# Performance work log

Hardware: AMD Instinct MI355X
Metric: run time of the kernel (lower is better)

Reference implementation:

```python
import jax, jax.numpy as jnp
import numpy as np

N = 100000   # nodes
E = 1600000  # edges
G = 64       # graphs
D = 64       # latent_dim
NF = 128     # num_node_feats
EF = 32      # num_edge_feats
NV = 5000    # num_node_val_feats
LV = 3       # max_lv
EPS = 1e-5


def setup_inputs() -> dict:
    key = jax.random.key(0)
    ks = jax.random.split(key, 16)
    s = 0.05
    return {
        "node_feat": jax.random.normal(ks[0], (N, NF), jnp.float32),
        "edge_feat": jax.random.normal(ks[1], (E, EF), jnp.float32),
        "w_n2l_W": jax.random.normal(ks[2], (NF, D), jnp.float32) * s,
        "w_n2l_b": jnp.zeros((D,), jnp.float32),
        "node_val_embedding": jax.random.normal(ks[3], (NV, D), jnp.float32) * s,
        "w_e2l_W": jax.random.normal(ks[4], (LV + 1, EF, D), jnp.float32) * s,
        "w_e2l_b": jnp.zeros((LV + 1, D), jnp.float32),
        "conv_W": jax.random.normal(ks[5], (LV, D, D), jnp.float32) * s,
        "conv_b": jnp.zeros((LV, D), jnp.float32),
        "l2_W": jax.random.normal(ks[6], (LV, D, D), jnp.float32) * s,
        "l2_b": jnp.zeros((LV, D), jnp.float32),
        "msg_g": jnp.ones((LV + 1, D), jnp.float32),
        "msg_b": jnp.zeros((LV + 1, D), jnp.float32),
        "hid_g": jnp.ones((LV, D), jnp.float32),
        "hid_b": jnp.zeros((LV, D), jnp.float32),
        "out_W": jax.random.normal(ks[7], (D, D), jnp.float32) * s,
        "out_b": jnp.zeros((D,), jnp.float32),
        "edge_from": jax.random.randint(ks[8], (E,), 0, N, jnp.int32),
        "edge_to": jax.random.randint(ks[9], (E,), 0, N, jnp.int32),
        "g_idx": jnp.sort(jax.random.randint(ks[10], (N,), 0, G, jnp.int32)),
        "node_val_idx": jax.random.randint(ks[11], (N,), 0, NV, jnp.int32),
    }


def _bn(x, g, b):
    # BatchNorm1d in training mode: biased batch stats
    m = jnp.mean(x, axis=0)
    v = jnp.mean(jnp.square(x - m), axis=0)
    return (x - m) * jax.lax.rsqrt(v + EPS) * g + b


def reference(node_feat, edge_feat, w_n2l_W, w_n2l_b, node_val_embedding,
              w_e2l_W, w_e2l_b, conv_W, conv_b, l2_W, l2_b,
              msg_g, msg_b, hid_g, hid_b, out_W, out_b,
              edge_from, edge_to, g_idx, node_val_idx):
    act = jax.nn.relu
    # input node transform + sparse node-value embedding (one-hot spmm == gather)
    h = node_feat @ w_n2l_W + w_n2l_b + node_val_embedding[node_val_idx]
    # edge->node pool for level 0
    e0 = edge_feat @ w_e2l_W[0] + w_e2l_b[0]
    h = h + jax.ops.segment_sum(e0, edge_to, num_segments=N)
    h = _bn(act(h), msg_g[0], msg_b[0])
    for lv in range(LV):
        # MessagePassing with add-aggr: gather sources, scatter-add to targets, then Linear
        agg = jax.ops.segment_sum(h[edge_from], edge_to, num_segments=N)
        node_linear = agg @ conv_W[lv] + conv_b[lv]
        e = edge_feat @ w_e2l_W[lv + 1] + w_e2l_b[lv + 1]
        merged = act(node_linear + jax.ops.segment_sum(e, edge_to, num_segments=N))
        merged = _bn(merged, hid_g[lv], hid_b[lv])
        h = _bn(act(merged @ l2_W[lv] + l2_b[lv] + h), msg_g[lv + 1], msg_b[lv + 1])
    # readout: gnn_out='last', readout_agg='max', act_last=True, bn=False
    pooled = jax.ops.segment_max(h, g_idx, num_segments=G)
    return act(pooled @ out_W + out_b)
```

## Files before the change

kernel.cpp:

```cpp
#include <hip/hip_runtime.h>
#include <math.h>

#define NN 100000
#define EE 1600000
#define GG 64
#define DD 64
#define NF 128
#define EF 32
#define LVL 3
#define EPSBN 1e-5f
#define NTILES ((NN + 63) / 64)
#define NBKT 391

typedef unsigned short u16;
typedef unsigned int u32;
typedef unsigned long long u64;
typedef short s4v __attribute__((ext_vector_type(4)));
typedef short bf16x8 __attribute__((ext_vector_type(8)));
typedef float f32x4 __attribute__((ext_vector_type(4)));

__device__ __forceinline__ float4 ld4(const float* p) { return *(const float4*)p; }
__device__ __forceinline__ u16 f2b(float f) {
    u32 u = __float_as_uint(f);
    return (u16)((u + 0x7FFFu + ((u >> 16) & 1u)) >> 16);
}
__device__ __forceinline__ float b2f(u16 u) { return __uint_as_float(((u32)u) << 16); }
__device__ __forceinline__ float blo(u32 u) { return __uint_as_float(u << 16); }
__device__ __forceinline__ float bhi(u32 u) { return __uint_as_float(u & 0xFFFF0000u); }

__global__ void k1b(const int* __restrict__ to, int* __restrict__ bhist) {
    __shared__ int h[NBKT];
    for (int i = threadIdx.x; i < NBKT; i += 256) h[i] = 0;
    __syncthreads();
    for (int e = blockIdx.x * 256 + threadIdx.x; e < EE; e += 256 * gridDim.x)
        atomicAdd(&h[to[e] >> 8], 1);
    __syncthreads();
    for (int i = threadIdx.x; i < NBKT; i += 256)
        if (h[i]) atomicAdd(&bhist[i], h[i]);
}

__global__ void k1c(const int* __restrict__ bhist, int* __restrict__ bbase,
                    int* __restrict__ gcur) {
    __shared__ int s[512];
    int t = threadIdx.x;
    s[t] = (t < NBKT) ? bhist[t] : 0;
    __syncthreads();
    for (int off = 1; off < 512; off <<= 1) {
        int v = (t >= off) ? s[t - off] : 0;
        __syncthreads();
        s[t] += v;
        __syncthreads();
    }
    if (t < NBKT) {
        int base = t ? s[t - 1] : 0;
        bbase[t] = base;
        gcur[t] = base;
    }
    if (t == NBKT - 1) bbase[NBKT] = s[t];
}

__global__ void k1d(const int* __restrict__ to, const int* __restrict__ from,
                    int* __restrict__ gcur, int2* __restrict__ tmp) {
    __shared__ int h[NBKT];
    __shared__ int cur[NBKT];
    for (int i = threadIdx.x; i < NBKT; i += 256) h[i] = 0;
    __syncthreads();
    for (int e = blockIdx.x * 256 + threadIdx.x; e < EE; e += 256 * gridDim.x)
        atomicAdd(&h[to[e] >> 8], 1);
    __syncthreads();
    for (int i = threadIdx.x; i < NBKT; i += 256)
        cur[i] = h[i] ? atomicAdd(&gcur[i], h[i]) : 0;
    __syncthreads();
    for (int e = blockIdx.x * 256 + threadIdx.x; e < EE; e += 256 * gridDim.x) {
        int tt = to[e];
        int b = tt >> 8;
        int pos = atomicAdd(&cur[b], 1);
        tmp[pos] = make_int2(from[e] | ((tt & 255) << 17), e);
    }
}

__global__ void kp2(const int2* __restrict__ tmp, const int* __restrict__ bbase,
                    int* __restrict__ row_ptr, int* __restrict__ src_s,
                    int* __restrict__ eid_s) {
    __shared__ int s[256];
    __shared__ int cur[256];
    int b = blockIdx.x, t = threadIdx.x;
    int e0 = bbase[b], e1 = bbase[b + 1];
    s[t] = 0;
    __syncthreads();
    for (int e = e0 + t; e < e1; e += 256) atomicAdd(&s[(tmp[e].x >> 17) & 255], 1);
    __syncthreads();
    int v = s[t];
    for (int off = 1; off < 256; off <<= 1) {
        int u = (t >= off) ? s[t - off] : 0;
        __syncthreads();
        s[t] += u;
        __syncthreads();
    }
    int excl = e0 + s[t] - v;
    cur[t] = excl;
    int n = b * 256 + t;
    if (n < NN) row_ptr[n] = excl;
    if (b == NBKT - 1 && t == 0) row_ptr[NN] = e1;
    __syncthreads();
    for (int e = e0 + t; e < e1; e += 256) {
        int2 w = tmp[e];
        int pos = atomicAdd(&cur[(w.x >> 17) & 255], 1);
        src_s[pos] = w.x & 0x1FFFF;
        eid_s[pos] = w.y;
    }
}

__global__ void kpool(const float* __restrict__ ef, const int* __restrict__ row_ptr,
                      const int* __restrict__ eid_s, u16* __restrict__ pooled) {
    int lane = threadIdx.x & 63;
    int wid = threadIdx.x >> 6;
    int w = lane & 15, slot = lane >> 4;
    for (int n = blockIdx.x * 4 + wid; n < NN; n += gridDim.x * 4) {
        int e0 = row_ptr[n], e1 = row_ptr[n + 1];
        float ax = 0.f, ay = 0.f;
        int e = e0 + slot;
        for (; e + 12 < e1; e += 16) {
            int i0 = eid_s[e], i1 = eid_s[e + 4], i2 = eid_s[e + 8], i3 = eid_s[e + 12];
            float2 v0 = *(const float2*)(ef + (size_t)i0 * EF + 2 * w);
            float2 v1 = *(const float2*)(ef + (size_t)i1 * EF + 2 * w);
            float2 v2 = *(const float2*)(ef + (size_t)i2 * EF + 2 * w);
            float2 v3 = *(const float2*)(ef + (size_t)i3 * EF + 2 * w);
            ax += (v0.x + v1.x) + (v2.x + v3.x);
            ay += (v0.y + v1.y) + (v2.y + v3.y);
        }
        for (; e < e1; e += 4) {
            float2 v = *(const float2*)(ef + (size_t)eid_s[e] * EF + 2 * w);
            ax += v.x;
            ay += v.y;
        }
        ax += __shfl_xor(ax, 16);
        ax += __shfl_xor(ax, 32);
        ay += __shfl_xor(ay, 16);
        ay += __shfl_xor(ay, 32);
        if (slot == 0) {
            u32 o = (u32)f2b(ax) | ((u32)f2b(ay) << 16);
            *(u32*)&pooled[(size_t)n * EF + 2 * w] = o;
        }
    }
}

template <int K1, int K2, bool A1BF, bool AAFF, bool EMB, bool BE, bool RESID>
__global__ __launch_bounds__(256) void kgemm_mfma(
    const void* __restrict__ A1v, const u16* __restrict__ A2,
    const float* __restrict__ W1, const float* __restrict__ W2,
    const float* __restrict__ bias, const float* __restrict__ be,
    const int* __restrict__ row_ptr, const float* __restrict__ emb,
    const int* __restrict__ nvi, const u16* __restrict__ resid,
    const float* __restrict__ raff, const float* __restrict__ aaff,
    u16* __restrict__ Xb, float* __restrict__ stats) {
    constexpr int K = K1 + K2;
    constexpr int KP = K + 8;
    __shared__ u16 A_lds[64 * KP];
    __shared__ u16 Wt_lds[64 * KP];
    __shared__ float red[128];

    const int t = threadIdx.x;
    const int lane = t & 63;
    const int wv = t >> 6;
    const int l15 = lane & 15;
    const int lg = lane >> 4;

    for (int idx = t; idx < K * 16; idx += 256) {
        int k = idx >> 4, c4 = (idx & 15) * 4;
        float4 w4 = (k < K1) ? ld4(W1 + (size_t)k * 64 + c4)
                             : ld4(W2 + (size_t)(k - K1) * 64 + c4);
        Wt_lds[(c4 + 0) * KP + k] = f2b(w4.x);
        Wt_lds[(c4 + 1) * KP + k] = f2b(w4.y);
        Wt_lds[(c4 + 2) * KP + k] = f2b(w4.z);
        Wt_lds[(c4 + 3) * KP + k] = f2b(w4.w);
    }
    if (t < 128) red[t] = 0.f;

    float bias_c[4], be_c[4], rsc_c[4], rsh_c[4];
#pragma unroll
    for (int n = 0; n < 4; n++) {
        int ch = 16 * n + l15;
        bias_c[n] = bias[ch];
        be_c[n] = BE ? be[ch] : 0.f;
        rsc_c[n] = RESID ? raff[ch] : 0.f;
        rsh_c[n] = RESID ? raff[64 + ch] : 0.f;
    }

    for (int tile = blockIdx.x; tile < NTILES; tile += gridDim.x) {
        int nb = tile * 64;
        __syncthreads();
        if (A1BF) {
            const u16* A1b = (const u16*)A1v;
            for (int idx = t; idx < 64 * (K1 / 4); idx += 256) {
                int node = idx / (K1 / 4), kq = (idx % (K1 / 4)) * 4;
                int gn = nb + node;
                s4v v = {0, 0, 0, 0};
                if (gn < NN) {
                    v = *(const s4v*)(A1b + (size_t)gn * K1 + kq);
                    if (AAFF) {
#pragma unroll
                        for (int i = 0; i < 4; i++) {
                            float f = b2f((u16)v[i]) * aaff[kq + i] + aaff[64 + kq + i];
                            v[i] = (short)f2b(f);
                        }
                    }
                }
                *(s4v*)&A_lds[node * KP + kq] = v;
            }
        } else {
            const float* A1f = (const float*)A1v;
            for (int idx = t; idx < 64 * (K1 / 4); idx += 256) {
                int node = idx / (K1 / 4), kq = (idx % (K1 / 4)) * 4;
                int gn = nb + node;
                s4v v = {0, 0, 0, 0};
                if (gn < NN) {
                    float4 a = ld4(A1f + (size_t)gn * K1 + kq);
                    v[0] = (short)f2b(a.x); v[1] = (short)f2b(a.y);
                    v[2] = (short)f2b(a.z); v[3] = (short)f2b(a.w);
                }
                *(s4v*)&A_lds[node * KP + kq] = v;
            }
        }
        if (K2 > 0) {
            for (int idx = t; idx < 64 * (K2 / 4); idx += 256) {
                int node = idx / (K2 / 4), kq = (idx % (K2 / 4)) * 4;
                int gn = nb + node;
                s4v v = {0, 0, 0, 0};
                if (gn < NN) v = *(const s4v*)(A2 + (size_t)gn * K2 + kq);
                *(s4v*)&A_lds[node * KP + K1 + kq] = v;
            }
        }
        __syncthreads();

        f32x4 acc[4];
#pragma unroll
        for (int n = 0; n < 4; n++) acc[n] = (f32x4){0.f, 0.f, 0.f, 0.f};
        const int arow = 16 * wv + l15;
#pragma unroll
        for (int kk = 0; kk < K; kk += 32) {
            s4v alo = *(const s4v*)&A_lds[arow * KP + kk + lg * 4];
            s4v ahi = *(const s4v*)&A_lds[arow * KP + kk + lg * 4 + 16];
            bf16x8 a = __builtin_shufflevector(alo, ahi, 0, 1, 2, 3, 4, 5, 6, 7);
#pragma unroll
            for (int n = 0; n < 4; n++) {
                s4v wlo = *(const s4v*)&Wt_lds[(16 * n + l15) * KP + kk + lg * 4];
                s4v whi = *(const s4v*)&Wt_lds[(16 * n + l15) * KP + kk + lg * 4 + 16];
                bf16x8 b = __builtin_shufflevector(wlo, whi, 0, 1, 2, 3, 4, 5, 6, 7);
                acc[n] = __builtin_amdgcn_mfma_f32_16x16x32_bf16(a, b, acc[n], 0, 0, 0);
            }
        }

        float ss[4] = {0, 0, 0, 0}, sq2[4] = {0, 0, 0, 0};
#pragma unroll
        for (int r = 0; r < 4; r++) {
            int node = nb + 16 * wv + lg * 4 + r;
            if (node < NN) {
                float deg = BE ? (float)(row_ptr[node + 1] - row_ptr[node]) : 0.f;
                int nv = EMB ? nvi[node] : 0;
#pragma unroll
                for (int n = 0; n < 4; n++) {
                    int ch = 16 * n + l15;
                    float v = acc[n][r] + bias_c[n];
                    if (BE) v += deg * be_c[n];
                    if (EMB) v += emb[(size_t)nv * 64 + ch];
                    if (RESID) v += b2f(resid[(size_t)node * 64 + ch]) * rsc_c[n] + rsh_c[n];
                    v = fmaxf(v, 0.f);
                    Xb[(size_t)node * 64 + ch] = f2b(v);
                    ss[n] += v;
                    sq2[n] += v * v;
                }
            }
        }
#pragma unroll
        for (int n = 0; n < 4; n++) {
            float a = ss[n];
            a += __shfl_xor(a, 16);
            a += __shfl_xor(a, 32);
            float b = sq2[n];
            b += __shfl_xor(b, 16);
            b += __shfl_xor(b, 32);
            if (lg == 0) {
                atomicAdd(&red[16 * n + l15], a);
                atomicAdd(&red[64 + 16 * n + l15], b);
            }
        }
    }
    __syncthreads();
    if (t < 128) atomicAdd(&stats[t], red[t]);
}

__global__ void kfin(float* __restrict__ stats, const float* __restrict__ g,
                     const float* __restrict__ b, int slot) {
    int t = threadIdx.x;
    float mean = stats[t] * (1.0f / NN);
    float var = stats[64 + t] * (1.0f / NN) - mean * mean;
    float rstd = rsqrtf(fmaxf(var, 0.f) + EPSBN);
    float sc = g[t] * rstd;
    float* slotp = stats + 128 + slot * 128;
    slotp[t] = sc;
    slotp[64 + t] = b[t] - mean * sc;
    stats[t] = 0.f;
    stats[64 + t] = 0.f;
}

__global__ void kmsg_bf(const u64* __restrict__ h4, const int* __restrict__ row_ptr,
                        const int* __restrict__ src_s, const float* __restrict__ aff,
                        u64* __restrict__ agg) {
    int lane = threadIdx.x & 63;
    int wid = threadIdx.x >> 6;
    int w = lane & 15, slot = lane >> 4;
    float sc0 = aff[4 * w], sc1 = aff[4 * w + 1];
    float sc2 = aff[4 * w + 2], sc3 = aff[4 * w + 3];
    float sh0 = aff[64 + 4 * w], sh1 = aff[64 + 4 * w + 1];
    float sh2 = aff[64 + 4 * w + 2], sh3 = aff[64 + 4 * w + 3];
    for (int n = blockIdx.x * 4 + wid; n < NN; n += gridDim.x * 4) {
        int e0 = row_ptr[n], e1 = row_ptr[n + 1];
        float a0 = 0.f, a1 = 0.f, a2 = 0.f, a3 = 0.f;
        int e = e0 + slot;
        for (; e + 12 < e1; e += 16) {
            int s0 = src_s[e], s1 = src_s[e + 4], s2 = src_s[e + 8], s3 = src_s[e + 12];
            u64 v0 = h4[(size_t)s0 * 16 + w];
            u64 v1 = h4[(size_t)s1 * 16 + w];
            u64 v2 = h4[(size_t)s2 * 16 + w];
            u64 v3 = h4[(size_t)s3 * 16 + w];
            u32 l0 = (u32)v0, h0 = (u32)(v0 >> 32);
            u32 l1 = (u32)v1, h1 = (u32)(v1 >> 32);
            u32 l2 = (u32)v2, h2w = (u32)(v2 >> 32);
            u32 l3 = (u32)v3, h3 = (u32)(v3 >> 32);
            a0 += (blo(l0) + blo(l1)) + (blo(l2) + blo(l3));
            a1 += (bhi(l0) + bhi(l1)) + (bhi(l2) + bhi(l3));
            a2 += (blo(h0) + blo(h1)) + (blo(h2w) + blo(h3));
            a3 += (bhi(h0) + bhi(h1)) + (bhi(h2w) + bhi(h3));
        }
        for (; e < e1; e += 4) {
            u64 v = h4[(size_t)src_s[e] * 16 + w];
            u32 l = (u32)v, h = (u32)(v >> 32);
            a0 += blo(l);
            a1 += bhi(l);
            a2 += blo(h);
            a3 += bhi(h);
        }
        a0 += __shfl_xor(a0, 16);
        a0 += __shfl_xor(a0, 32);
        a1 += __shfl_xor(a1, 16);
        a1 += __shfl_xor(a1, 32);
        a2 += __shfl_xor(a2, 16);
        a2 += __shfl_xor(a2, 32);
        a3 += __shfl_xor(a3, 16);
        a3 += __shfl_xor(a3, 32);
        if (slot == 0) {
            float deg = (float)(e1 - e0);
            u32 lo = (u32)f2b(sc0 * a0 + deg * sh0) | ((u32)f2b(sc1 * a1 + deg * sh1) << 16);
            u32 hi = (u32)f2b(sc2 * a2 + deg * sh2) | ((u32)f2b(sc3 * a3 + deg * sh3) << 16);
            agg[(size_t)n * 16 + w] = (u64)lo | ((u64)hi << 32);
        }
    }
}

__device__ __forceinline__ unsigned fenc(float f) {
    unsigned u = __float_as_uint(f);
    return (u >> 31) ? ~u : (u | 0x80000000u);
}
__device__ __forceinline__ float fdec(unsigned k) {
    return (k >> 31) ? __uint_as_float(k ^ 0x80000000u) : __uint_as_float(~k);
}

__global__ void kinitpk(unsigned* __restrict__ pk) {
    int i = blockIdx.x * blockDim.x + threadIdx.x;
    if (i < GG * DD) pk[i] = 0x007FFFFFu;
}

__global__ void kread(const u16* __restrict__ h2, const int* __restrict__ gidx,
                      const float* __restrict__ aff, unsigned* __restrict__ pk) {
    int lane = threadIdx.x & 63;
    int wid = threadIdx.x >> 6;
    float sc = aff[lane], sh = aff[64 + lane];
    int gw = blockIdx.x * 4 + wid;
    int nw = gridDim.x * 4;
    int chunk = (NN + nw - 1) / nw;
    int lo = gw * chunk, hi = min(lo + chunk, NN);
    if (lo >= hi) return;
    int cur = gidx[lo];
    float acc = -INFINITY;
    for (int n = lo; n < hi; n++) {
        int g = gidx[n];
        if (g != cur) {
            atomicMax(&pk[cur * DD + lane], fenc(acc));
            cur = g;
            acc = -INFINITY;
        }
        acc = fmaxf(acc, b2f(h2[(size_t)n * 64 + lane]) * sc + sh);
    }
    atomicMax(&pk[cur * DD + lane], fenc(acc));
}

__global__ void kout(const unsigned* __restrict__ pk, const float* __restrict__ W,
                     const float* __restrict__ b, float* __restrict__ out) {
    int t = blockIdx.x * blockDim.x + threadIdx.x;
    int g = t >> 6, d = t & 63;
    float acc = b[d];
    for (int k = 0; k < DD; k++) {
        float p = fdec(pk[g * DD + k]);
        acc += p * W[k * DD + d];
    }
    out[t] = fmaxf(acc, 0.f);
}

extern "C" void kernel_launch(void* const* d_in, const int* in_sizes, int n_in,
                              void* d_out, int out_size, void* d_ws, size_t ws_size,
                              hipStream_t stream) {
    const float* node_feat = (const float*)d_in[0];
    const float* edge_feat = (const float*)d_in[1];
    const float* w_n2l_W = (const float*)d_in[2];
    const float* w_n2l_b = (const float*)d_in[3];
    const float* nve = (const float*)d_in[4];
    const float* w_e2l_W = (const float*)d_in[5];
    const float* w_e2l_b = (const float*)d_in[6];
    const float* conv_W = (const float*)d_in[7];
    const float* conv_b = (const float*)d_in[8];
    const float* l2_W = (const float*)d_in[9];
    const float* l2_b = (const float*)d_in[10];
    const float* msg_g = (const float*)d_in[11];
    const float* msg_b = (const float*)d_in[12];
    const float* hid_g = (const float*)d_in[13];
    const float* hid_b = (const float*)d_in[14];
    const float* out_W = (const float*)d_in[15];
    const float* out_b = (const float*)d_in[16];
    const int* edge_from = (const int*)d_in[17];
    const int* edge_to = (const int*)d_in[18];
    const int* g_idx = (const int*)d_in[19];
    const int* nvi = (const int*)d_in[20];
    float* out = (float*)d_out;

    char* ws = (char*)d_ws;
    size_t off = 0;
    auto alloc = [&](size_t bytes) -> void* {
        void* p = ws + off;
        off += (bytes + 255) / 256 * 256;
        return p;
    };
    int* row_ptr = (int*)alloc((size_t)(NN + 1) * 4);
    int* src_s = (int*)alloc((size_t)EE * 4);
    int* eid_s = (int*)alloc((size_t)EE * 4);
    int2* tmp = (int2*)alloc((size_t)EE * 8);
    u16* pooled_ef = (u16*)alloc((size_t)NN * EF * 2);
    u16* h2a = (u16*)alloc((size_t)NN * DD * 2);
    u16* h2b = (u16*)alloc((size_t)NN * DD * 2);
    u16* agg_bf = (u16*)alloc((size_t)NN * DD * 2);
    u16* mb_bf = (u16*)alloc((size_t)NN * DD * 2);
    float* stats = (float*)alloc(1024 * 4);
    unsigned* pk = (unsigned*)alloc((size_t)GG * DD * 4);
    int* bhist = (int*)alloc((size_t)NBKT * 4);
    int* bbase = (int*)alloc((size_t)(NBKT + 1) * 4);
    int* gcur = (int*)alloc((size_t)NBKT * 4);
    (void)ws_size; (void)n_in; (void)in_sizes; (void)out_size;

    hipMemsetAsync(bhist, 0, (size_t)NBKT * 4, stream);
    hipMemsetAsync(stats, 0, 1024 * 4, stream);
    kinitpk<<<16, 256, 0, stream>>>(pk);

    k1b<<<256, 256, 0, stream>>>(edge_to, bhist);
    k1c<<<1, 512, 0, stream>>>(bhist, bbase, gcur);
    k1d<<<256, 256, 0, stream>>>(edge_to, edge_from, gcur, tmp);
    kp2<<<NBKT, 256, 0, stream>>>(tmp, bbase, row_ptr, src_s, eid_s);
    kpool<<<4096, 256, 0, stream>>>(edge_feat, row_ptr, eid_s, pooled_ef);

    const int GB = 782;

    kgemm_mfma<NF, EF, false, false, true, true, false>
        <<<GB, 256, 0, stream>>>(node_feat, pooled_ef, w_n2l_W, w_e2l_W,
                                 w_n2l_b, w_e2l_b, row_ptr, nve, nvi,
                                 nullptr, nullptr, nullptr, h2a, stats);
    kfin<<<1, 64, 0, stream>>>(stats, msg_g, msg_b, 0);

    u16* hcur = h2a;
    u16* hnext = h2b;
    for (int lv = 0; lv < LVL; lv++) {
        kmsg_bf<<<4096, 256, 0, stream>>>((const u64*)hcur, row_ptr, src_s,
                                          stats + 128 + lv * 128, (u64*)agg_bf);
        kgemm_mfma<DD, EF, true, false, false, true, false>
            <<<GB, 256, 0, stream>>>(agg_bf, pooled_ef, conv_W + lv * DD * DD,
                                     w_e2l_W + (size_t)(lv + 1) * EF * DD,
                                     conv_b + lv * DD,
                                     w_e2l_b + (size_t)(lv + 1) * DD, row_ptr,
                                     nullptr, nullptr, nullptr, nullptr, nullptr,
                                     mb_bf, stats);
        kfin<<<1, 64, 0, stream>>>(stats, hid_g + lv * DD, hid_b + lv * DD, 4 + lv);
        kgemm_mfma<DD, 0, true, true, false, false, true>
            <<<GB, 256, 0, stream>>>(mb_bf, nullptr, l2_W + lv * DD * DD, nullptr,
                                     l2_b + lv * DD, nullptr, row_ptr, nullptr,
                                     nullptr, hcur, stats + 128 + lv * 128,
                                     stats + 128 + (4 + lv) * 128, hnext, stats);
        kfin<<<1, 64, 0, stream>>>(stats, msg_g + (lv + 1) * DD, msg_b + (lv + 1) * DD,
                                   lv + 1);
        u16* tmp2 = hcur; hcur = hnext; hnext = tmp2;
    }

    kread<<<1024, 256, 0, stream>>>(hcur, g_idx, stats + 128 + LVL * 128, pk);
    kout<<<GG, 64, 0, stream>>>(pk, out_W, out_b, out);
}
```

Measured before the change: 586.3 us.

## Fuse edge-feature pooling into CSR build and fold BN finalize into consumers

The CSR construction now copies each edge's features, converted to bf16, into bucket order. The second pass then pools them per node right after sorting, which removes the separate kpool kernel and its random gathers of edge features. The seven kfin launches are gone: each consumer (kmsg_bf, the GEMM's residual and input affine, kread) computes BN scale and shift directly from per-slot accumulated stats. The cost is a large 100MB temporary buffer, extra write traffic in k1d, and a serial per-thread pooling loop in kp2 whose load is uneven across nodes.

```diff
diff --git a/kernel.cpp b/kernel.cpp
--- a/kernel.cpp
+++ b/kernel.cpp
@@ -24,9 +24,21 @@
     u32 u = __float_as_uint(f);
     return (u16)((u + 0x7FFFu + ((u >> 16) & 1u)) >> 16);
 }
+__device__ __forceinline__ u32 pk2(float x, float y) {
+    return (u32)f2b(x) | ((u32)f2b(y) << 16);
+}
 __device__ __forceinline__ float b2f(u16 u) { return __uint_as_float(((u32)u) << 16); }
 __device__ __forceinline__ float blo(u32 u) { return __uint_as_float(u << 16); }
 __device__ __forceinline__ float bhi(u32 u) { return __uint_as_float(u & 0xFFFF0000u); }
+
+__device__ __forceinline__ float2 bn_pair(const float* __restrict__ slot,
+                                          const float* __restrict__ g,
+                                          const float* __restrict__ b, int ch) {
+    float mean = slot[ch] * (1.0f / NN);
+    float var = slot[64 + ch] * (1.0f / NN) - mean * mean;
+    float sc = g[ch] * rsqrtf(fmaxf(var, 0.f) + EPSBN);
+    return make_float2(sc, b[ch] - mean * sc);
+}
 
 __global__ void k1b(const int* __restrict__ to, int* __restrict__ bhist) {
     __shared__ int h[NBKT];
@@ -60,7 +72,8 @@
 }
 
 __global__ void k1d(const int* __restrict__ to, const int* __restrict__ from,
-                    int* __restrict__ gcur, int2* __restrict__ tmp) {
+                    const float* __restrict__ ef, int* __restrict__ gcur,
+                    int* __restrict__ tmpw, uint4* __restrict__ tmp_ef) {
     __shared__ int h[NBKT];
     __shared__ int cur[NBKT];
     for (int i = threadIdx.x; i < NBKT; i += 256) h[i] = 0;
@@ -75,20 +88,29 @@
         int tt = to[e];
         int b = tt >> 8;
         int pos = atomicAdd(&cur[b], 1);
-        tmp[pos] = make_int2(from[e] | ((tt & 255) << 17), e);
-    }
-}
-
-__global__ void kp2(const int2* __restrict__ tmp, const int* __restrict__ bbase,
-                    int* __restrict__ row_ptr, int* __restrict__ src_s,
-                    int* __restrict__ eid_s) {
+        tmpw[pos] = from[e] | ((tt & 255) << 17);
+        const float4* efp = (const float4*)(ef + (size_t)e * EF);
+        uint4* dst = tmp_ef + (size_t)pos * 4;
+#pragma unroll
+        for (int j = 0; j < 4; j++) {
+            float4 a = efp[2 * j], b4 = efp[2 * j + 1];
+            dst[j] = make_uint4(pk2(a.x, a.y), pk2(a.z, a.w), pk2(b4.x, b4.y),
+                                pk2(b4.z, b4.w));
+        }
+    }
+}
+
+__global__ void kp2(const int* __restrict__ tmpw, const uint4* __restrict__ tmp_ef,
+                    const int* __restrict__ bbase, int* __restrict__ row_ptr,
+                    int* __restrict__ src_s, int* __restrict__ perm,
+                    u16* __restrict__ pooled) {
     __shared__ int s[256];
     __shared__ int cur[256];
     int b = blockIdx.x, t = threadIdx.x;
     int e0 = bbase[b], e1 = bbase[b + 1];
     s[t] = 0;
     __syncthreads();
-    for (int e = e0 + t; e < e1; e += 256) atomicAdd(&s[(tmp[e].x >> 17) & 255], 1);
+    for (int e = e0 + t; e < e1; e += 256) atomicAdd(&s[(tmpw[e] >> 17) & 255], 1);
     __syncthreads();
     int v = s[t];
     for (int off = 1; off < 256; off <<= 1) {
@@ -104,44 +126,38 @@
     if (b == NBKT - 1 && t == 0) row_ptr[NN] = e1;
     __syncthreads();
     for (int e = e0 + t; e < e1; e += 256) {
-        int2 w = tmp[e];
-        int pos = atomicAdd(&cur[(w.x >> 17) & 255], 1);
-        src_s[pos] = w.x & 0x1FFFF;
-        eid_s[pos] = w.y;
-    }
-}
-
-__global__ void kpool(const float* __restrict__ ef, const int* __restrict__ row_ptr,
-                      const int* __restrict__ eid_s, u16* __restrict__ pooled) {
-    int lane = threadIdx.x & 63;
-    int wid = threadIdx.x >> 6;
-    int w = lane & 15, slot = lane >> 4;
-    for (int n = blockIdx.x * 4 + wid; n < NN; n += gridDim.x * 4) {
-        int e0 = row_ptr[n], e1 = row_ptr[n + 1];
-        float ax = 0.f, ay = 0.f;
-        int e = e0 + slot;
-        for (; e + 12 < e1; e += 16) {
-            int i0 = eid_s[e], i1 = eid_s[e + 4], i2 = eid_s[e + 8], i3 = eid_s[e + 12];
-            float2 v0 = *(const float2*)(ef + (size_t)i0 * EF + 2 * w);
-            float2 v1 = *(const float2*)(ef + (size_t)i1 * EF + 2 * w);
-            float2 v2 = *(const float2*)(ef + (size_t)i2 * EF + 2 * w);
-            float2 v3 = *(const float2*)(ef + (size_t)i3 * EF + 2 * w);
-            ax += (v0.x + v1.x) + (v2.x + v3.x);
-            ay += (v0.y + v1.y) + (v2.y + v3.y);
-        }
-        for (; e < e1; e += 4) {
-            float2 v = *(const float2*)(ef + (size_t)eid_s[e] * EF + 2 * w);
-            ax += v.x;
-            ay += v.y;
-        }
-        ax += __shfl_xor(ax, 16);
-        ax += __shfl_xor(ax, 32);
-        ay += __shfl_xor(ay, 16);
-        ay += __shfl_xor(ay, 32);
-        if (slot == 0) {
-            u32 o = (u32)f2b(ax) | ((u32)f2b(ay) << 16);
-            *(u32*)&pooled[(size_t)n * EF + 2 * w] = o;
-        }
+        int w = tmpw[e];
+        int pos = atomicAdd(&cur[(w >> 17) & 255], 1);
+        src_s[pos] = w & 0x1FFFF;
+        perm[pos] = e;
+    }
+    __threadfence_block();
+    __syncthreads();
+    if (n < NN) {
+        float av[EF];
+#pragma unroll
+        for (int c = 0; c < EF; c++) av[c] = 0.f;
+        for (int i = 0; i < v; i++) {
+            int e = perm[excl + i];
+            const uint4* p = tmp_ef + (size_t)e * 4;
+            uint4 q0 = p[0], q1 = p[1], q2 = p[2], q3 = p[3];
+            av[0] += blo(q0.x); av[1] += bhi(q0.x); av[2] += blo(q0.y); av[3] += bhi(q0.y);
+            av[4] += blo(q0.z); av[5] += bhi(q0.z); av[6] += blo(q0.w); av[7] += bhi(q0.w);
+            av[8] += blo(q1.x); av[9] += bhi(q1.x); av[10] += blo(q1.y); av[11] += bhi(q1.y);
+            av[12] += blo(q1.z); av[13] += bhi(q1.z); av[14] += blo(q1.w); av[15] += bhi(q1.w);
+            av[16] += blo(q2.x); av[17] += bhi(q2.x); av[18] += blo(q2.y); av[19] += bhi(q2.y);
+            av[20] += blo(q2.z); av[21] += bhi(q2.z); av[22] += blo(q2.w); av[23] += bhi(q2.w);
+            av[24] += blo(q3.x); av[25] += bhi(q3.x); av[26] += blo(q3.y); av[27] += bhi(q3.y);
+            av[28] += blo(q3.z); av[29] += bhi(q3.z); av[30] += blo(q3.w); av[31] += bhi(q3.w);
+        }
+        u32 orow[16];
+#pragma unroll
+        for (int j = 0; j < 16; j++) orow[j] = pk2(av[2 * j], av[2 * j + 1]);
+        uint4* pr = (uint4*)((u32*)pooled + (size_t)n * 16);
+        pr[0] = make_uint4(orow[0], orow[1], orow[2], orow[3]);
+        pr[1] = make_uint4(orow[4], orow[5], orow[6], orow[7]);
+        pr[2] = make_uint4(orow[8], orow[9], orow[10], orow[11]);
+        pr[3] = make_uint4(orow[12], orow[13], orow[14], orow[15]);
     }
 }
 
@@ -152,13 +168,16 @@
     const float* __restrict__ bias, const float* __restrict__ be,
     const int* __restrict__ row_ptr, const float* __restrict__ emb,
     const int* __restrict__ nvi, const u16* __restrict__ resid,
-    const float* __restrict__ raff, const float* __restrict__ aaff,
+    const float* __restrict__ rslot, const float* __restrict__ rg,
+    const float* __restrict__ rb, const float* __restrict__ aslot,
+    const float* __restrict__ ag, const float* __restrict__ ab,
     u16* __restrict__ Xb, float* __restrict__ stats) {
     constexpr int K = K1 + K2;
     constexpr int KP = K + 8;
     __shared__ u16 A_lds[64 * KP];
     __shared__ u16 Wt_lds[64 * KP];
     __shared__ float red[128];
+    __shared__ float affl[128];
 
     const int t = threadIdx.x;
     const int lane = t & 63;
@@ -176,6 +195,11 @@
         Wt_lds[(c4 + 3) * KP + k] = f2b(w4.w);
     }
     if (t < 128) red[t] = 0.f;
+    if (AAFF && t < 64) {
+        float2 p = bn_pair(aslot, ag, ab, t);
+        affl[t] = p.x;
+        affl[64 + t] = p.y;
+    }
 
     float bias_c[4], be_c[4], rsc_c[4], rsh_c[4];
 #pragma unroll
@@ -183,8 +207,14 @@
         int ch = 16 * n + l15;
         bias_c[n] = bias[ch];
         be_c[n] = BE ? be[ch] : 0.f;
-        rsc_c[n] = RESID ? raff[ch] : 0.f;
-        rsh_c[n] = RESID ? raff[64 + ch] : 0.f;
+        if (RESID) {
+            float2 p = bn_pair(rslot, rg, rb, ch);
+            rsc_c[n] = p.x;
+            rsh_c[n] = p.y;
+        } else {
+            rsc_c[n] = 0.f;
+            rsh_c[n] = 0.f;
+        }
     }
 
     for (int tile = blockIdx.x; tile < NTILES; tile += gridDim.x) {
@@ -201,7 +231,7 @@
                     if (AAFF) {
 #pragma unroll
                         for (int i = 0; i < 4; i++) {
-                            float f = b2f((u16)v[i]) * aaff[kq + i] + aaff[64 + kq + i];
+                            float f = b2f((u16)v[i]) * affl[kq + i] + affl[64 + kq + i];
                             v[i] = (short)f2b(f);
                         }
                     }
@@ -290,34 +320,21 @@
     if (t < 128) atomicAdd(&stats[t], red[t]);
 }
 
-__global__ void kfin(float* __restrict__ stats, const float* __restrict__ g,
-                     const float* __restrict__ b, int slot) {
-    int t = threadIdx.x;
-    float mean = stats[t] * (1.0f / NN);
-    float var = stats[64 + t] * (1.0f / NN) - mean * mean;
-    float rstd = rsqrtf(fmaxf(var, 0.f) + EPSBN);
-    float sc = g[t] * rstd;
-    float* slotp = stats + 128 + slot * 128;
-    slotp[t] = sc;
-    slotp[64 + t] = b[t] - mean * sc;
-    stats[t] = 0.f;
-    stats[64 + t] = 0.f;
-}
-
 __global__ void kmsg_bf(const u64* __restrict__ h4, const int* __restrict__ row_ptr,
-                        const int* __restrict__ src_s, const float* __restrict__ aff,
+                        const int* __restrict__ src_s, const float* __restrict__ slot,
+                        const float* __restrict__ g, const float* __restrict__ bb,
                         u64* __restrict__ agg) {
     int lane = threadIdx.x & 63;
     int wid = threadIdx.x >> 6;
-    int w = lane & 15, slot = lane >> 4;
-    float sc0 = aff[4 * w], sc1 = aff[4 * w + 1];
-    float sc2 = aff[4 * w + 2], sc3 = aff[4 * w + 3];
-    float sh0 = aff[64 + 4 * w], sh1 = aff[64 + 4 * w + 1];
-    float sh2 = aff[64 + 4 * w + 2], sh3 = aff[64 + 4 * w + 3];
+    int w = lane & 15, sl = lane >> 4;
+    float2 p0 = bn_pair(slot, g, bb, 4 * w);
+    float2 p1 = bn_pair(slot, g, bb, 4 * w + 1);
+    float2 p2 = bn_pair(slot, g, bb, 4 * w + 2);
+    float2 p3 = bn_pair(slot, g, bb, 4 * w + 3);
     for (int n = blockIdx.x * 4 + wid; n < NN; n += gridDim.x * 4) {
         int e0 = row_ptr[n], e1 = row_ptr[n + 1];
         float a0 = 0.f, a1 = 0.f, a2 = 0.f, a3 = 0.f;
-        int e = e0 + slot;
+        int e = e0 + sl;
         for (; e + 12 < e1; e += 16) {
             int s0 = src_s[e], s1 = src_s[e + 4], s2 = src_s[e + 8], s3 = src_s[e + 12];
             u64 v0 = h4[(size_t)s0 * 16 + w];
@@ -349,10 +366,10 @@
         a2 += __shfl_xor(a2, 32);
         a3 += __shfl_xor(a3, 16);
         a3 += __shfl_xor(a3, 32);
-        if (slot == 0) {
+        if (sl == 0) {
             float deg = (float)(e1 - e0);
-            u32 lo = (u32)f2b(sc0 * a0 + deg * sh0) | ((u32)f2b(sc1 * a1 + deg * sh1) << 16);
-            u32 hi = (u32)f2b(sc2 * a2 + deg * sh2) | ((u32)f2b(sc3 * a3 + deg * sh3) << 16);
+            u32 lo = pk2(p0.x * a0 + deg * p0.y, p1.x * a1 + deg * p1.y);
+            u32 hi = pk2(p2.x * a2 + deg * p2.y, p3.x * a3 + deg * p3.y);
             agg[(size_t)n * 16 + w] = (u64)lo | ((u64)hi << 32);
         }
     }
@@ -372,10 +389,12 @@
 }
 
 __global__ void kread(const u16* __restrict__ h2, const int* __restrict__ gidx,
-                      const float* __restrict__ aff, unsigned* __restrict__ pk) {
+                      const float* __restrict__ slot, const float* __restrict__ g,
+                      const float* __restrict__ bb, unsigned* __restrict__ pk) {
     int lane = threadIdx.x & 63;
     int wid = threadIdx.x >> 6;
-    float sc = aff[lane], sh = aff[64 + lane];
+    float2 p = bn_pair(slot, g, bb, lane);
+    float sc = p.x, sh = p.y;
     int gw = blockIdx.x * 4 + wid;
     int nw = gridDim.x * 4;
     int chunk = (NN + nw - 1) / nw;
@@ -384,10 +403,10 @@
     int cur = gidx[lo];
     float acc = -INFINITY;
     for (int n = lo; n < hi; n++) {
-        int g = gidx[n];
-        if (g != cur) {
+        int gg = gidx[n];
+        if (gg != cur) {
             atomicMax(&pk[cur * DD + lane], fenc(acc));
-            cur = g;
+            cur = gg;
             acc = -INFINITY;
         }
         acc = fmaxf(acc, b2f(h2[(size_t)n * 64 + lane]) * sc + sh);
@@ -442,8 +461,9 @@
     };
     int* row_ptr = (int*)alloc((size_t)(NN + 1) * 4);
     int* src_s = (int*)alloc((size_t)EE * 4);
-    int* eid_s = (int*)alloc((size_t)EE * 4);
-    int2* tmp = (int2*)alloc((size_t)EE * 8);
+    int* perm = (int*)alloc((size_t)EE * 4);
+    int* tmpw = (int*)alloc((size_t)EE * 4);
+    uint4* tmp_ef = (uint4*)alloc((size_t)EE * 64);
     u16* pooled_ef = (u16*)alloc((size_t)NN * EF * 2);
     u16* h2a = (u16*)alloc((size_t)NN * DD * 2);
     u16* h2b = (u16*)alloc((size_t)NN * DD * 2);
@@ -462,41 +482,43 @@
 
     k1b<<<256, 256, 0, stream>>>(edge_to, bhist);
     k1c<<<1, 512, 0, stream>>>(bhist, bbase, gcur);
-    k1d<<<256, 256, 0, stream>>>(edge_to, edge_from, gcur, tmp);
-    kp2<<<NBKT, 256, 0, stream>>>(tmp, bbase, row_ptr, src_s, eid_s);
-    kpool<<<4096, 256, 0, stream>>>(edge_feat, row_ptr, eid_s, pooled_ef);
+    k1d<<<512, 256, 0, stream>>>(edge_to, edge_from, edge_feat, gcur, tmpw, tmp_ef);
+    kp2<<<NBKT, 256, 0, stream>>>(tmpw, tmp_ef, bbase, row_ptr, src_s, perm, pooled_ef);
 
     const int GB = 782;
+    const float* S = stats;
 
     kgemm_mfma<NF, EF, false, false, true, true, false>
         <<<GB, 256, 0, stream>>>(node_feat, pooled_ef, w_n2l_W, w_e2l_W,
-                                 w_n2l_b, w_e2l_b, row_ptr, nve, nvi,
-                                 nullptr, nullptr, nullptr, h2a, stats);
-    kfin<<<1, 64, 0, stream>>>(stats, msg_g, msg_b, 0);
+                                 w_n2l_b, w_e2l_b, row_ptr, nve, nvi, nullptr,
+                                 nullptr, nullptr, nullptr, nullptr, nullptr, nullptr,
+                                 h2a, stats + 0 * 128);
 
     u16* hcur = h2a;
     u16* hnext = h2b;
     for (int lv = 0; lv < LVL; lv++) {
         kmsg_bf<<<4096, 256, 0, stream>>>((const u64*)hcur, row_ptr, src_s,
-                                          stats + 128 + lv * 128, (u64*)agg_bf);
+                                          S + lv * 128, msg_g + lv * 64, msg_b + lv * 64,
+                                          (u64*)agg_bf);
         kgemm_mfma<DD, EF, true, false, false, true, false>
             <<<GB, 256, 0, stream>>>(agg_bf, pooled_ef, conv_W + lv * DD * DD,
                                      w_e2l_W + (size_t)(lv + 1) * EF * DD,
                                      conv_b + lv * DD,
                                      w_e2l_b + (size_t)(lv + 1) * DD, row_ptr,
                                      nullptr, nullptr, nullptr, nullptr, nullptr,
-                                     mb_bf, stats);
-        kfin<<<1, 64, 0, stream>>>(stats, hid_g + lv * DD, hid_b + lv * DD, 4 + lv);
+                                     nullptr, nullptr, nullptr, nullptr,
+                                     mb_bf, stats + (4 + lv) * 128);
         kgemm_mfma<DD, 0, true, true, false, false, true>
             <<<GB, 256, 0, stream>>>(mb_bf, nullptr, l2_W + lv * DD * DD, nullptr,
                                      l2_b + lv * DD, nullptr, row_ptr, nullptr,
-                                     nullptr, hcur, stats + 128 + lv * 128,
-                                     stats + 128 + (4 + lv) * 128, hnext, stats);
-        kfin<<<1, 64, 0, stream>>>(stats, msg_g + (lv + 1) * DD, msg_b + (lv + 1) * DD,
-                                   lv + 1);
-        u16* tmp2 = hcur; hcur = hnext; hnext = tmp2;
-    }
-
-    kread<<<1024, 256, 0, stream>>>(hcur, g_idx, stats + 128 + LVL * 128, pk);
+                                     nullptr, hcur,
+                                     S + lv * 128, msg_g + lv * 64, msg_b + lv * 64,
+                                     S + (4 + lv) * 128, hid_g + lv * 64, hid_b + lv * 64,
+                                     hnext, stats + (lv + 1) * 128);
+        u16* tsw = hcur; hcur = hnext; hnext = tsw;
+    }
+
+    kread<<<1024, 256, 0, stream>>>(hcur, g_idx, S + LVL * 128, msg_g + LVL * 64,
+                                    msg_b + LVL * 64, pk);
     kout<<<GG, 64, 0, stream>>>(pk, out_W, out_b, out);
 }
```

Result: slower. 626.4 us (+6.8%).
